# Performance work log

Hardware: AMD Instinct MI355X
Metric: run time of the kernel (lower is better)

## Reference

```python
import jax, jax.numpy as jnp
import numpy as np

N_NODES = 50000
N_EDGES = 800000
IN_C, HID_C, OUT_C = 128, 128, 64


def setup_inputs() -> dict:
    key = jax.random.key(0)
    ks = jax.random.split(key, 12)
    glorot = lambda k, shape: jax.random.normal(k, shape, dtype=jnp.float32) * (2.0 / (shape[0] + shape[-1])) ** 0.5
    return {
        "x": jax.random.normal(ks[0], (N_NODES, IN_C), dtype=jnp.float32),
        "edge_index": jax.random.randint(ks[1], (2, N_EDGES), 0, N_NODES, dtype=jnp.int64),
        "W_s1": glorot(ks[2], (IN_C, HID_C)), "b_s1": jnp.zeros((HID_C,), jnp.float32),
        "W_s2": glorot(ks[3], (HID_C, HID_C)), "b_s2": jnp.zeros((HID_C,), jnp.float32),
        "W_m1": glorot(ks[4], (IN_C, HID_C)), "b_m1": jnp.zeros((HID_C,), jnp.float32),
        "W_m21": glorot(ks[5], (IN_C, HID_C)), "b_m21": jnp.zeros((HID_C,), jnp.float32),
        "W_m22": glorot(ks[6], (HID_C, HID_C)), "b_m22": jnp.zeros((HID_C,), jnp.float32),
        "W_att": glorot(ks[7], (HID_C, 1)), "b_att": jnp.zeros((1,), jnp.float32),
        "W_fc": glorot(ks[8], (2 * HID_C, OUT_C)), "b_fc": jnp.zeros((OUT_C,), jnp.float32),
    }


def _gcn_conv(x, W, b, src, dst, n_nodes):
    """PyG GCNConv: add self-loops, symmetric deg^-1/2 norm, linear, scatter-add, bias."""
    xw = x @ W  # [N, H]
    loop = jnp.arange(n_nodes, dtype=src.dtype)
    s = jnp.concatenate([src, loop])
    d = jnp.concatenate([dst, loop])
    ones = jnp.ones(s.shape[0], dtype=x.dtype)
    deg = jax.ops.segment_sum(ones, d, num_segments=n_nodes)  # in-degree incl. self loop
    dinv = jnp.where(deg > 0, jax.lax.rsqrt(deg), 0.0)
    norm = dinv[s] * dinv[d]  # [E+N]
    msg = xw[s] * norm[:, None]
    return jax.ops.segment_sum(msg, d, num_segments=n_nodes) + b


def reference(x, edge_index, W_s1, b_s1, W_s2, b_s2, W_m1, b_m1, W_m21, b_m21,
              W_m22, b_m22, W_att, b_att, W_fc, b_fc):
    n = x.shape[0]
    src, dst = edge_index[0], edge_index[1]
    # structural branch: two GCN layers
    h_struct = jax.nn.relu(_gcn_conv(x, W_s1, b_s1, src, dst, n))
    h_struct = jax.nn.relu(_gcn_conv(h_struct, W_s2, b_s2, src, dst, n))
    # meta branches
    h1 = jax.nn.relu(_gcn_conv(x, W_m1, b_m1, src, dst, n))
    h2 = jax.nn.relu(_gcn_conv(x, W_m21, b_m21, src, dst, n))
    h2 = jax.nn.relu(_gcn_conv(h2, W_m22, b_m22, src, dst, n))
    # attention-weighted fusion over the 2 branches
    H = jnp.stack([h1, h2], axis=1)  # [N, 2, H]
    attn_scores = H @ W_att + b_att  # [N, 2, 1]
    attn_weights = jax.nn.softmax(attn_scores, axis=1)
    h_meta = jnp.sum(attn_weights * H, axis=1)  # [N, H]
    h_comb = jnp.concatenate([h_struct, h_meta], axis=1)  # [N, 2H]
    return h_comb @ W_fc + b_fc  # [N, OUT_C]
```

## Files before the change

### kernel.cpp

```cpp
#include <hip/hip_runtime.h>
#include <hip/hip_bf16.h>

#define N_NODES 50000
#define N_EDGES 800000
#define IN_C 128
#define HID_C 128
#define OUT_C 64

#define SCAN_BS 256
#define SCAN_NB ((N_NODES + SCAN_BS - 1) / SCAN_BS)

#define PREP_CVT_NB   6250
#define PREP_DEG_NB   3125
#define PREP_WCAT_NB  192
#define PREP_TP_NB    64
#define PREP_NB (PREP_CVT_NB + PREP_DEG_NB + PREP_WCAT_NB + 3 * PREP_TP_NB)

typedef __attribute__((ext_vector_type(8))) short bf16x8;
typedef __attribute__((ext_vector_type(4))) float f32x4;

__device__ __forceinline__ ushort f2bf(float f) {
    unsigned u = __float_as_uint(f);
    return (ushort)((u + 0x7fffu + ((u >> 16) & 1u)) >> 16);
}
__device__ __forceinline__ float bf2f(ushort u) {
    return __uint_as_float(((unsigned)u) << 16);
}

__global__ __launch_bounds__(256)
void prep_kernel(const float* __restrict__ x, uint2* __restrict__ xb4,
                 const int* __restrict__ edst, int* __restrict__ hist,
                 const float* __restrict__ Ws1, const float* __restrict__ Wm21,
                 const float* __restrict__ Wm1,
                 const float* __restrict__ bs1, const float* __restrict__ bm21,
                 const float* __restrict__ bm1,
                 ushort* __restrict__ Wcat_t, float* __restrict__ bcat,
                 const float* __restrict__ Ws2, ushort* __restrict__ Ws2t,
                 const float* __restrict__ Wm22, ushort* __restrict__ Wm22t,
                 const float* __restrict__ Wfc, ushort* __restrict__ Wfct,
                 int* __restrict__ row_ptr) {
    const int bid = blockIdx.x;
    const int t = threadIdx.x;
    if (bid < PREP_CVT_NB) {
        int i = bid * 256 + t;
        float4 v = *(const float4*)&x[(size_t)i * 4];
        uint2 o;
        o.x = (uint)f2bf(v.x) | ((uint)f2bf(v.y) << 16);
        o.y = (uint)f2bf(v.z) | ((uint)f2bf(v.w) << 16);
        xb4[i] = o;
    } else if (bid < PREP_CVT_NB + PREP_DEG_NB) {
        int e = (bid - PREP_CVT_NB) * 256 + t;
        atomicAdd(&hist[edst[e]], 1);
    } else if (bid < PREP_CVT_NB + PREP_DEG_NB + PREP_WCAT_NB) {
        int idx = (bid - PREP_CVT_NB - PREP_DEG_NB) * 256 + t;
        int c = idx >> 7, k = idx & 127;
        float v = (c < 128) ? Ws1[k * 128 + c]
                : (c < 256) ? Wm21[k * 128 + (c - 128)]
                            : Wm1[k * 128 + (c - 256)];
        Wcat_t[idx] = f2bf(v);
        if (idx < 384) {
            bcat[idx] = (idx < 128) ? bs1[idx] : (idx < 256) ? bm21[idx - 128] : bm1[idx - 256];
        }
        if (idx == 0) row_ptr[N_NODES] = N_EDGES;
    } else if (bid < PREP_CVT_NB + PREP_DEG_NB + PREP_WCAT_NB + PREP_TP_NB) {
        int idx = (bid - PREP_CVT_NB - PREP_DEG_NB - PREP_WCAT_NB) * 256 + t;
        int c = idx >> 7, k = idx & 127;
        Ws2t[idx] = f2bf(Ws2[(size_t)k * 128 + c]);
    } else if (bid < PREP_CVT_NB + PREP_DEG_NB + PREP_WCAT_NB + 2 * PREP_TP_NB) {
        int idx = (bid - PREP_CVT_NB - PREP_DEG_NB - PREP_WCAT_NB - PREP_TP_NB) * 256 + t;
        int c = idx >> 7, k = idx & 127;
        Wm22t[idx] = f2bf(Wm22[(size_t)k * 128 + c]);
    } else {
        int idx = (bid - PREP_CVT_NB - PREP_DEG_NB - PREP_WCAT_NB - 2 * PREP_TP_NB) * 256 + t;
        int c = idx >> 8, k = idx & 255;
        Wfct[idx] = f2bf(Wfc[(size_t)k * 64 + c]);
    }
}

__global__ __launch_bounds__(SCAN_BS)
void scan1_kernel(const int* __restrict__ hist, int* __restrict__ bsum,
                  float* __restrict__ dinv, int n) {
    __shared__ int s[SCAN_BS];
    int t = threadIdx.x;
    int i = blockIdx.x * SCAN_BS + t;
    int v = (i < n) ? hist[i] : 0;
    if (i < n) dinv[i] = rsqrtf((float)(v + 1));
    s[t] = v;
    __syncthreads();
#pragma unroll
    for (int off = SCAN_BS / 2; off > 0; off >>= 1) {
        if (t < off) s[t] += s[t + off];
        __syncthreads();
    }
    if (t == 0) bsum[blockIdx.x] = s[0];
}

__global__ __launch_bounds__(SCAN_BS)
void scan3_kernel(const int* __restrict__ hist, const int* __restrict__ bsum,
                  int* __restrict__ row_ptr, int* __restrict__ cursor, int n) {
    __shared__ int s[SCAN_BS];
    __shared__ int pre_s;
    int t = threadIdx.x;
    int b = blockIdx.x;
    int p = 0;
    for (int j = t; j < b; j += SCAN_BS) p += bsum[j];
    s[t] = p;
    __syncthreads();
#pragma unroll
    for (int off = SCAN_BS / 2; off > 0; off >>= 1) {
        if (t < off) s[t] += s[t + off];
        __syncthreads();
    }
    if (t == 0) pre_s = s[0];
    __syncthreads();
    const int pre = pre_s;
    __syncthreads();
    int i = b * SCAN_BS + t;
    int v = (i < n) ? hist[i] : 0;
    s[t] = v;
    __syncthreads();
#pragma unroll
    for (int off = 1; off < SCAN_BS; off <<= 1) {
        int tmp = (t >= off) ? s[t - off] : 0;
        __syncthreads();
        s[t] += tmp;
        __syncthreads();
    }
    if (i < n) {
        int ex = s[t] - v + pre;
        row_ptr[i] = ex;
        cursor[i]  = ex;
    }
}

__global__ void fill_kernel(const int* __restrict__ src, const int* __restrict__ dst, int E,
                            int* __restrict__ cursor, int2* __restrict__ edge_data,
                            const float* __restrict__ dinv) {
    int e = blockIdx.x * blockDim.x + threadIdx.x;
    if (e < E) {
        int d = dst[e];
        int s = src[e];
        int pos = atomicAdd(&cursor[d], 1);
        edge_data[pos] = make_int2(s, __float_as_int(dinv[s]));
    }
}

template<int C>
__global__ __launch_bounds__(256)
void agg_bf16(const ushort* __restrict__ X, int ldx,
              ushort* __restrict__ Y, int ldy,
              const int* __restrict__ row_ptr,
              const int2* __restrict__ edge_data,
              const float* __restrict__ dinv, int n) {
    constexpr int CG = C / 8;
    constexpr int SLOTS = 64 / CG;
    const int wid = blockIdx.x * (blockDim.x >> 6) + (threadIdx.x >> 6);
    if (wid >= n) return;
    const int lane = threadIdx.x & 63;
    const int cg = lane & (CG - 1);
    const int slot = lane / CG;

    const float di = dinv[wid];
    float acc[8] = {0.f, 0.f, 0.f, 0.f, 0.f, 0.f, 0.f, 0.f};

    auto fma_row = [&](uint4 v, float w) {
        acc[0] = fmaf(w, __uint_as_float(v.x << 16), acc[0]);
        acc[1] = fmaf(w, __uint_as_float(v.x & 0xffff0000u), acc[1]);
        acc[2] = fmaf(w, __uint_as_float(v.y << 16), acc[2]);
        acc[3] = fmaf(w, __uint_as_float(v.y & 0xffff0000u), acc[3]);
        acc[4] = fmaf(w, __uint_as_float(v.z << 16), acc[4]);
        acc[5] = fmaf(w, __uint_as_float(v.z & 0xffff0000u), acc[5]);
        acc[6] = fmaf(w, __uint_as_float(v.w << 16), acc[6]);
        acc[7] = fmaf(w, __uint_as_float(v.w & 0xffff0000u), acc[7]);
    };

    if (slot == 0) {
        uint4 v = *(const uint4*)&X[(size_t)wid * ldx + cg * 8];
        fma_row(v, di * di);
    }
    const int e0 = row_ptr[wid], e1 = row_ptr[wid + 1];
    int e = e0 + slot;
    for (; e + 3 * SLOTS < e1; e += 4 * SLOTS) {
        const int2 d0 = edge_data[e];
        const int2 d1 = edge_data[e + SLOTS];
        const int2 d2 = edge_data[e + 2 * SLOTS];
        const int2 d3 = edge_data[e + 3 * SLOTS];
        const uint4 v0 = *(const uint4*)&X[(size_t)d0.x * ldx + cg * 8];
        const uint4 v1 = *(const uint4*)&X[(size_t)d1.x * ldx + cg * 8];
        const uint4 v2 = *(const uint4*)&X[(size_t)d2.x * ldx + cg * 8];
        const uint4 v3 = *(const uint4*)&X[(size_t)d3.x * ldx + cg * 8];
        fma_row(v0, di * __int_as_float(d0.y));
        fma_row(v1, di * __int_as_float(d1.y));
        fma_row(v2, di * __int_as_float(d2.y));
        fma_row(v3, di * __int_as_float(d3.y));
    }
    for (; e < e1; e += SLOTS) {
        const int2 d0 = edge_data[e];
        const uint4 v0 = *(const uint4*)&X[(size_t)d0.x * ldx + cg * 8];
        fma_row(v0, di * __int_as_float(d0.y));
    }
#pragma unroll
    for (int j = 0; j < 8; ++j) {
        if (SLOTS == 4) acc[j] += __shfl_xor(acc[j], 16);
        if (SLOTS >= 2) acc[j] += __shfl_xor(acc[j], 32);
    }
    if (slot == 0) {
        uint4 o;
        o.x = (uint)f2bf(acc[0]) | ((uint)f2bf(acc[1]) << 16);
        o.y = (uint)f2bf(acc[2]) | ((uint)f2bf(acc[3]) << 16);
        o.z = (uint)f2bf(acc[4]) | ((uint)f2bf(acc[5]) << 16);
        o.w = (uint)f2bf(acc[6]) | ((uint)f2bf(acc[7]) << 16);
        *(uint4*)&Y[(size_t)wid * ldy + cg * 8] = o;
    }
}

__global__ __launch_bounds__(256)
void mfma_gemm_kernel(const ushort* __restrict__ A, int lda,
                      const ushort* __restrict__ Wt,
                      const float* __restrict__ bias,
                      void* __restrict__ Yv, int ldy,
                      int M, int relu, int obf16) {
    __shared__ char Asmem[128 * 272];
    const int tid = threadIdx.x;
    const int lane = tid & 63;
    const int w = tid >> 6;
    const int rb = blockIdx.x * 128;
    const int cb = blockIdx.y * 128;

    {
        const int rowbase = tid >> 4;
        const int inrow = (tid & 15) * 8;
#pragma unroll
        for (int it = 0; it < 8; ++it) {
            int row = it * 16 + rowbase;
            uint4 v = make_uint4(0u, 0u, 0u, 0u);
            int r = rb + row;
            if (r < M) v = *(const uint4*)&A[(size_t)r * lda + inrow];
            *(uint4*)&Asmem[row * 272 + (tid & 15) * 16] = v;
        }
    }
    __syncthreads();

    f32x4 acc[2][8];
#pragma unroll
    for (int i = 0; i < 2; ++i)
#pragma unroll
        for (int j = 0; j < 8; ++j) acc[i][j] = (f32x4){0.f, 0.f, 0.f, 0.f};

    const int arow0 = w * 32 + (lane & 15);
    const int kq = (lane >> 4) * 8;
    const int ccol = lane & 15;
#pragma unroll
    for (int ks = 0; ks < 4; ++ks) {
        const int k0 = ks * 32;
        const bf16x8 a0 = *(const bf16x8*)&Asmem[arow0 * 272 + (k0 + kq) * 2];
        const bf16x8 a1 = *(const bf16x8*)&Asmem[(arow0 + 16) * 272 + (k0 + kq) * 2];
#pragma unroll
        for (int ct = 0; ct < 8; ++ct) {
            const bf16x8 b = *(const bf16x8*)&Wt[(size_t)(cb + ct * 16 + ccol) * 128 + k0 + kq];
            acc[0][ct] = __builtin_amdgcn_mfma_f32_16x16x32_bf16(a0, b, acc[0][ct], 0, 0, 0);
            acc[1][ct] = __builtin_amdgcn_mfma_f32_16x16x32_bf16(a1, b, acc[1][ct], 0, 0, 0);
        }
    }

    const int rowq = (lane >> 4) * 4;
#pragma unroll
    for (int rt = 0; rt < 2; ++rt) {
#pragma unroll
        for (int ct = 0; ct < 8; ++ct) {
            const int col = cb + ct * 16 + ccol;
            const float bcol = bias[col];
#pragma unroll
            for (int r = 0; r < 4; ++r) {
                const int row = rb + w * 32 + rt * 16 + rowq + r;
                if (row >= M) continue;
                float v = acc[rt][ct][r] + bcol;
                if (relu) v = fmaxf(v, 0.f);
                if (obf16) ((ushort*)Yv)[(size_t)row * ldy + col] = f2bf(v);
                else       ((float*)Yv)[(size_t)row * ldy + col] = v;
            }
        }
    }
}

__global__ __launch_bounds__(256)
void gemm2_kernel(const ushort* __restrict__ bufB,
                  const ushort* __restrict__ Ws2t, const float* __restrict__ bs2,
                  const ushort* __restrict__ Wm22t, const float* __restrict__ bm22,
                  const ushort* __restrict__ cat1,
                  const float* __restrict__ Watt, const float* __restrict__ batt,
                  ushort* __restrict__ comb, int M) {
    __shared__ char Asmem[128 * 272];
    const int tid = threadIdx.x;
    const int lane = tid & 63;
    const int w = tid >> 6;
    const int rb = blockIdx.x * 128;
    const int branch = blockIdx.y;
    const ushort* A = bufB + (branch ? 128 : 0);
    const ushort* Wt = branch ? Wm22t : Ws2t;
    const float* bias = branch ? bm22 : bs2;

    {
        const int rowbase = tid >> 4;
        const int seg = tid & 15;
#pragma unroll
        for (int it = 0; it < 8; ++it) {
            int row = it * 16 + rowbase;
            uint4 v = make_uint4(0u, 0u, 0u, 0u);
            int r = rb + row;
            if (r < M) v = *(const uint4*)&A[(size_t)r * 256 + seg * 8];
            *(uint4*)&Asmem[row * 272 + seg * 16] = v;
        }
    }
    __syncthreads();

    f32x4 acc[2][8];
#pragma unroll
    for (int i = 0; i < 2; ++i)
#pragma unroll
        for (int j = 0; j < 8; ++j) acc[i][j] = (f32x4){0.f, 0.f, 0.f, 0.f};

    const int arow0 = w * 32 + (lane & 15);
    const int kq = (lane >> 4) * 8;
    const int ccol = lane & 15;
#pragma unroll
    for (int ks = 0; ks < 4; ++ks) {
        const int k0 = ks * 32;
        const bf16x8 a0 = *(const bf16x8*)&Asmem[arow0 * 272 + (k0 + kq) * 2];
        const bf16x8 a1 = *(const bf16x8*)&Asmem[(arow0 + 16) * 272 + (k0 + kq) * 2];
#pragma unroll
        for (int ct = 0; ct < 8; ++ct) {
            const bf16x8 b = *(const bf16x8*)&Wt[(size_t)(ct * 16 + ccol) * 128 + k0 + kq];
            acc[0][ct] = __builtin_amdgcn_mfma_f32_16x16x32_bf16(a0, b, acc[0][ct], 0, 0, 0);
            acc[1][ct] = __builtin_amdgcn_mfma_f32_16x16x32_bf16(a1, b, acc[1][ct], 0, 0, 0);
        }
    }

    const int quad = lane >> 4;
    if (branch == 0) {
#pragma unroll
        for (int rt = 0; rt < 2; ++rt) {
#pragma unroll
            for (int ct = 0; ct < 8; ++ct) {
                const int col = ct * 16 + ccol;
                const float bcol = bias[col];
#pragma unroll
                for (int r = 0; r < 4; ++r) {
                    const int row = rb + w * 32 + rt * 16 + quad * 4 + r;
                    if (row >= M) continue;
                    comb[(size_t)row * 256 + col] = f2bf(fmaxf(acc[rt][ct][r] + bcol, 0.f));
                }
            }
        }
    } else {
#pragma unroll
        for (int rt = 0; rt < 2; ++rt)
#pragma unroll
            for (int ct = 0; ct < 8; ++ct) {
                const float bcol = bias[ct * 16 + ccol];
#pragma unroll
                for (int r = 0; r < 4; ++r)
                    acc[rt][ct][r] = fmaxf(acc[rt][ct][r] + bcol, 0.f);
            }
        float wv[8];
#pragma unroll
        for (int ct = 0; ct < 8; ++ct) wv[ct] = Watt[ct * 16 + ccol];
        const float ba = batt[0];
#pragma unroll
        for (int rt = 0; rt < 2; ++rt) {
#pragma unroll
            for (int r = 0; r < 4; ++r) {
                const int row0 = rb + w * 32 + rt * 16 + quad * 4 + r;
                const int rowc = (row0 < M) ? row0 : (M - 1);
                const ushort* h1row = &cat1[(size_t)rowc * 384 + 256];
                float bp = 0.f, ap = 0.f;
#pragma unroll
                for (int ct = 0; ct < 8; ++ct) {
                    bp += acc[rt][ct][r] * wv[ct];
                    ap += bf2f(h1row[ct * 16 + ccol]) * wv[ct];
                }
#pragma unroll
                for (int off = 1; off < 16; off <<= 1) {
                    bp += __shfl_xor(bp, off);
                    ap += __shfl_xor(ap, off);
                }
                const float a = ap + ba, b = bp + ba;
                const float m = fmaxf(a, b);
                const float ea = __expf(a - m), eb = __expf(b - m);
                const float inv = 1.f / (ea + eb);
                const float wa = ea * inv, wb = eb * inv;
                if (row0 < M) {
#pragma unroll
                    for (int ct = 0; ct < 8; ++ct) {
                        const float h1 = bf2f(h1row[ct * 16 + ccol]);
                        comb[(size_t)row0 * 256 + 128 + ct * 16 + ccol] =
                            f2bf(fmaf(wa, h1, wb * acc[rt][ct][r]));
                    }
                }
            }
        }
    }
}

__global__ __launch_bounds__(256)
void mfma_fc_kernel(const ushort* __restrict__ A,
                    const ushort* __restrict__ Wt,
                    const float* __restrict__ bias,
                    float* __restrict__ Y, int M) {
    __shared__ char Asmem[64 * 528];
    const int tid = threadIdx.x;
    const int lane = tid & 63;
    const int w = tid >> 6;
    const int rb = blockIdx.x * 64;

    {
        const int rowbase = tid >> 5;
        const int seg = (tid & 31);
#pragma unroll
        for (int it = 0; it < 8; ++it) {
            int row = it * 8 + rowbase;
            uint4 v = make_uint4(0u, 0u, 0u, 0u);
            int r = rb + row;
            if (r < M) v = *(const uint4*)&A[(size_t)r * 256 + seg * 8];
            *(uint4*)&Asmem[row * 528 + seg * 16] = v;
        }
    }
    __syncthreads();

    f32x4 acc[4];
#pragma unroll
    for (int j = 0; j < 4; ++j) acc[j] = (f32x4){0.f, 0.f, 0.f, 0.f};

    const int arow = w * 16 + (lane & 15);
    const int kq = (lane >> 4) * 8;
    const int ccol = lane & 15;
#pragma unroll
    for (int ks = 0; ks < 8; ++ks) {
        const int k0 = ks * 32;
        const bf16x8 a = *(const bf16x8*)&Asmem[arow * 528 + (k0 + kq) * 2];
#pragma unroll
        for (int ct = 0; ct < 4; ++ct) {
            const bf16x8 b = *(const bf16x8*)&Wt[(size_t)(ct * 16 + ccol) * 256 + k0 + kq];
            acc[ct] = __builtin_amdgcn_mfma_f32_16x16x32_bf16(a, b, acc[ct], 0, 0, 0);
        }
    }

    const int rowq = (lane >> 4) * 4;
#pragma unroll
    for (int ct = 0; ct < 4; ++ct) {
        const int col = ct * 16 + ccol;
        const float bcol = bias[col];
#pragma unroll
        for (int r = 0; r < 4; ++r) {
            const int row = rb + w * 16 + rowq + r;
            if (row < M) Y[(size_t)row * 64 + col] = acc[ct][r] + bcol;
        }
    }
}

extern "C" void kernel_launch(void* const* d_in, const int* in_sizes, int n_in,
                              void* d_out, int out_size, void* d_ws, size_t ws_size,
                              hipStream_t stream) {
    const int N = N_NODES, E = N_EDGES;
    const float* x     = (const float*)d_in[0];
    const int*   ei    = (const int*)d_in[1];
    const int*   esrc  = ei;
    const int*   edst  = ei + E;
    const float* W_s1  = (const float*)d_in[2];
    const float* b_s1  = (const float*)d_in[3];
    const float* W_s2  = (const float*)d_in[4];
    const float* b_s2  = (const float*)d_in[5];
    const float* W_m1  = (const float*)d_in[6];
    const float* b_m1  = (const float*)d_in[7];
    const float* W_m21 = (const float*)d_in[8];
    const float* b_m21 = (const float*)d_in[9];
    const float* W_m22 = (const float*)d_in[10];
    const float* b_m22 = (const float*)d_in[11];
    const float* W_att = (const float*)d_in[12];
    const float* b_att = (const float*)d_in[13];
    const float* W_fc  = (const float*)d_in[14];
    const float* b_fc  = (const float*)d_in[15];
    float* out = (float*)d_out;

    char* base = (char*)d_ws;
    size_t off = 0;
    auto take = [&](size_t nbytes) -> void* {
        void* p = base + off;
        off += (nbytes + 255) & ~(size_t)255;
        return p;
    };
    int*    hist      = (int*)take((size_t)N * 4);
    int*    cursor    = (int*)take((size_t)N * 4);
    int*    row_ptr   = (int*)take((size_t)(N + 1) * 4);
    int*    bsum      = (int*)take((size_t)SCAN_NB * 4);
    int2*   edge_data = (int2*)take((size_t)E * 8);
    float*  dinv      = (float*)take((size_t)N * 4);
    ushort* xb        = (ushort*)take((size_t)N * 128 * 2);
    ushort* agg_x     = (ushort*)take((size_t)N * 128 * 2);
    ushort* cat1      = (ushort*)take((size_t)N * 384 * 2);
    ushort* bufB      = (ushort*)take((size_t)N * 256 * 2);
    ushort* comb      = (ushort*)take((size_t)N * 256 * 2);
    ushort* Wcat_t    = (ushort*)take((size_t)384 * 128 * 2);
    ushort* Ws2_t     = (ushort*)take((size_t)128 * 128 * 2);
    ushort* Wm22_t    = (ushort*)take((size_t)128 * 128 * 2);
    ushort* Wfc_t     = (ushort*)take((size_t)64 * 256 * 2);
    float*  bcat      = (float*)take((size_t)384 * 4);

    hipMemsetAsync(hist, 0, (size_t)N * 4, stream);
    prep_kernel<<<PREP_NB, 256, 0, stream>>>(x, (uint2*)xb, edst, hist,
                                             W_s1, W_m21, W_m1, b_s1, b_m21, b_m1,
                                             Wcat_t, bcat, W_s2, Ws2_t, W_m22, Wm22_t,
                                             W_fc, Wfc_t, row_ptr);
    scan1_kernel<<<SCAN_NB, SCAN_BS, 0, stream>>>(hist, bsum, dinv, N);
    scan3_kernel<<<SCAN_NB, SCAN_BS, 0, stream>>>(hist, bsum, row_ptr, cursor, N);
    fill_kernel<<<(E + 255) / 256, 256, 0, stream>>>(esrc, edst, E, cursor, edge_data, dinv);

    agg_bf16<128><<<(N + 3) / 4, 256, 0, stream>>>(xb, 128, agg_x, 128, row_ptr, edge_data, dinv, N);
    dim3 gm384((N + 127) / 128, 3);
    mfma_gemm_kernel<<<gm384, 256, 0, stream>>>(agg_x, 128, Wcat_t, bcat, cat1, 384, N, 1, 1);
    agg_bf16<256><<<(N + 3) / 4, 256, 0, stream>>>(cat1, 384, bufB, 256, row_ptr, edge_data, dinv, N);
    dim3 gm2((N + 127) / 128, 2);
    gemm2_kernel<<<gm2, 256, 0, stream>>>(bufB, Ws2_t, b_s2, Wm22_t, b_m22,
                                          cat1, W_att, b_att, comb, N);
    mfma_fc_kernel<<<(N + 63) / 64, 256, 0, stream>>>(comb, Wfc_t, b_fc, out, N);
}
```

Before: 383.6 us.

## Fuse second-layer GEMMs, attention fusion and final FC into one kernel

Merges the two-branch second GEMM (with attention softmax fusion) and the final FC GEMM into a single 512-thread kernel. The combined bf16 activations stay in shared memory instead of being written to and re-read from a global comb buffer, which also removes one kernel launch. Each block now handles both branches with 8 waves and uses about 68KB of LDS, which lowers occupancy. The mfma_gemm kernel is also simplified to hardcode relu and bf16 output.

```diff
diff --git a/kernel.cpp b/kernel.cpp
--- a/kernel.cpp
+++ b/kernel.cpp
@@ -3,9 +3,6 @@
 
 #define N_NODES 50000
 #define N_EDGES 800000
-#define IN_C 128
-#define HID_C 128
-#define OUT_C 64
 
 #define SCAN_BS 256
 #define SCAN_NB ((N_NODES + SCAN_BS - 1) / SCAN_BS)
@@ -218,8 +215,7 @@
 void mfma_gemm_kernel(const ushort* __restrict__ A, int lda,
                       const ushort* __restrict__ Wt,
                       const float* __restrict__ bias,
-                      void* __restrict__ Yv, int ldy,
-                      int M, int relu, int obf16) {
+                      ushort* __restrict__ Y, int ldy, int M) {
     __shared__ char Asmem[128 * 272];
     const int tid = threadIdx.x;
     const int lane = tid & 63;
@@ -229,14 +225,14 @@
 
     {
         const int rowbase = tid >> 4;
-        const int inrow = (tid & 15) * 8;
+        const int seg = tid & 15;
 #pragma unroll
         for (int it = 0; it < 8; ++it) {
             int row = it * 16 + rowbase;
             uint4 v = make_uint4(0u, 0u, 0u, 0u);
             int r = rb + row;
-            if (r < M) v = *(const uint4*)&A[(size_t)r * lda + inrow];
-            *(uint4*)&Asmem[row * 272 + (tid & 15) * 16] = v;
+            if (r < M) v = *(const uint4*)&A[(size_t)r * lda + seg * 8];
+            *(uint4*)&Asmem[row * 272 + seg * 16] = v;
         }
     }
     __syncthreads();
@@ -274,60 +270,62 @@
             for (int r = 0; r < 4; ++r) {
                 const int row = rb + w * 32 + rt * 16 + rowq + r;
                 if (row >= M) continue;
-                float v = acc[rt][ct][r] + bcol;
-                if (relu) v = fmaxf(v, 0.f);
-                if (obf16) ((ushort*)Yv)[(size_t)row * ldy + col] = f2bf(v);
-                else       ((float*)Yv)[(size_t)row * ldy + col] = v;
+                Y[(size_t)row * ldy + col] = f2bf(fmaxf(acc[rt][ct][r] + bcol, 0.f));
             }
         }
     }
 }
 
-__global__ __launch_bounds__(256)
-void gemm2_kernel(const ushort* __restrict__ bufB,
-                  const ushort* __restrict__ Ws2t, const float* __restrict__ bs2,
-                  const ushort* __restrict__ Wm22t, const float* __restrict__ bm22,
-                  const ushort* __restrict__ cat1,
-                  const float* __restrict__ Watt, const float* __restrict__ batt,
-                  ushort* __restrict__ comb, int M) {
-    __shared__ char Asmem[128 * 272];
+__global__ __launch_bounds__(512, 4)
+void gemm2fc_kernel(const ushort* __restrict__ bufB,
+                    const ushort* __restrict__ Ws2t, const float* __restrict__ bs2,
+                    const ushort* __restrict__ Wm22t, const float* __restrict__ bm22,
+                    const ushort* __restrict__ cat1,
+                    const float* __restrict__ Watt, const float* __restrict__ batt,
+                    const ushort* __restrict__ Wfct, const float* __restrict__ bfc,
+                    float* __restrict__ Y, int M) {
+    __shared__ __align__(16) char smem[69632];
     const int tid = threadIdx.x;
+    const int rb = blockIdx.x * 128;
+
+    {
+        const int seg = tid & 15;
+        const int rowbase = tid >> 4;
+#pragma unroll
+        for (int it = 0; it < 8; ++it) {
+            int idx = it * 32 + rowbase;
+            int region = idx >> 7;
+            int row = idx & 127;
+            int r = rb + row;
+            uint4 v = make_uint4(0u, 0u, 0u, 0u);
+            if (r < M) v = *(const uint4*)&bufB[(size_t)r * 256 + region * 128 + seg * 8];
+            *(uint4*)&smem[region * 34816 + row * 272 + seg * 16] = v;
+        }
+    }
+    __syncthreads();
+
+    const int w = tid >> 6;
     const int lane = tid & 63;
-    const int w = tid >> 6;
-    const int rb = blockIdx.x * 128;
-    const int branch = blockIdx.y;
-    const ushort* A = bufB + (branch ? 128 : 0);
+    const int branch = w >> 2;
+    const int wl = w & 3;
+    const char* Areg = smem + branch * 34816;
     const ushort* Wt = branch ? Wm22t : Ws2t;
     const float* bias = branch ? bm22 : bs2;
 
-    {
-        const int rowbase = tid >> 4;
-        const int seg = tid & 15;
-#pragma unroll
-        for (int it = 0; it < 8; ++it) {
-            int row = it * 16 + rowbase;
-            uint4 v = make_uint4(0u, 0u, 0u, 0u);
-            int r = rb + row;
-            if (r < M) v = *(const uint4*)&A[(size_t)r * 256 + seg * 8];
-            *(uint4*)&Asmem[row * 272 + seg * 16] = v;
-        }
-    }
-    __syncthreads();
-
     f32x4 acc[2][8];
 #pragma unroll
     for (int i = 0; i < 2; ++i)
 #pragma unroll
         for (int j = 0; j < 8; ++j) acc[i][j] = (f32x4){0.f, 0.f, 0.f, 0.f};
 
-    const int arow0 = w * 32 + (lane & 15);
+    const int arow0 = wl * 32 + (lane & 15);
     const int kq = (lane >> 4) * 8;
     const int ccol = lane & 15;
 #pragma unroll
     for (int ks = 0; ks < 4; ++ks) {
         const int k0 = ks * 32;
-        const bf16x8 a0 = *(const bf16x8*)&Asmem[arow0 * 272 + (k0 + kq) * 2];
-        const bf16x8 a1 = *(const bf16x8*)&Asmem[(arow0 + 16) * 272 + (k0 + kq) * 2];
+        const bf16x8 a0 = *(const bf16x8*)&Areg[arow0 * 272 + (k0 + kq) * 2];
+        const bf16x8 a1 = *(const bf16x8*)&Areg[(arow0 + 16) * 272 + (k0 + kq) * 2];
 #pragma unroll
         for (int ct = 0; ct < 8; ++ct) {
             const bf16x8 b = *(const bf16x8*)&Wt[(size_t)(ct * 16 + ccol) * 128 + k0 + kq];
@@ -336,32 +334,18 @@
         }
     }
 
+#pragma unroll
+    for (int rt = 0; rt < 2; ++rt)
+#pragma unroll
+        for (int ct = 0; ct < 8; ++ct) {
+            const float bcol = bias[ct * 16 + ccol];
+#pragma unroll
+            for (int r = 0; r < 4; ++r)
+                acc[rt][ct][r] = fmaxf(acc[rt][ct][r] + bcol, 0.f);
+        }
+
     const int quad = lane >> 4;
-    if (branch == 0) {
-#pragma unroll
-        for (int rt = 0; rt < 2; ++rt) {
-#pragma unroll
-            for (int ct = 0; ct < 8; ++ct) {
-                const int col = ct * 16 + ccol;
-                const float bcol = bias[col];
-#pragma unroll
-                for (int r = 0; r < 4; ++r) {
-                    const int row = rb + w * 32 + rt * 16 + quad * 4 + r;
-                    if (row >= M) continue;
-                    comb[(size_t)row * 256 + col] = f2bf(fmaxf(acc[rt][ct][r] + bcol, 0.f));
-                }
-            }
-        }
-    } else {
-#pragma unroll
-        for (int rt = 0; rt < 2; ++rt)
-#pragma unroll
-            for (int ct = 0; ct < 8; ++ct) {
-                const float bcol = bias[ct * 16 + ccol];
-#pragma unroll
-                for (int r = 0; r < 4; ++r)
-                    acc[rt][ct][r] = fmaxf(acc[rt][ct][r] + bcol, 0.f);
-            }
+    if (branch == 1) {
         float wv[8];
 #pragma unroll
         for (int ct = 0; ct < 8; ++ct) wv[ct] = Watt[ct * 16 + ccol];
@@ -370,7 +354,7 @@
         for (int rt = 0; rt < 2; ++rt) {
 #pragma unroll
             for (int r = 0; r < 4; ++r) {
-                const int row0 = rb + w * 32 + rt * 16 + quad * 4 + r;
+                const int row0 = rb + wl * 32 + rt * 16 + quad * 4 + r;
                 const int rowc = (row0 < M) ? row0 : (M - 1);
                 const ushort* h1row = &cat1[(size_t)rowc * 384 + 256];
                 float bp = 0.f, ap = 0.f;
@@ -389,71 +373,52 @@
                 const float ea = __expf(a - m), eb = __expf(b - m);
                 const float inv = 1.f / (ea + eb);
                 const float wa = ea * inv, wb = eb * inv;
-                if (row0 < M) {
-#pragma unroll
-                    for (int ct = 0; ct < 8; ++ct) {
-                        const float h1 = bf2f(h1row[ct * 16 + ccol]);
-                        comb[(size_t)row0 * 256 + 128 + ct * 16 + ccol] =
-                            f2bf(fmaf(wa, h1, wb * acc[rt][ct][r]));
-                    }
+#pragma unroll
+                for (int ct = 0; ct < 8; ++ct) {
+                    const float h1 = bf2f(h1row[ct * 16 + ccol]);
+                    acc[rt][ct][r] = fmaf(wa, h1, wb * acc[rt][ct][r]);
                 }
             }
         }
     }
-}
-
-__global__ __launch_bounds__(256)
-void mfma_fc_kernel(const ushort* __restrict__ A,
-                    const ushort* __restrict__ Wt,
-                    const float* __restrict__ bias,
-                    float* __restrict__ Y, int M) {
-    __shared__ char Asmem[64 * 528];
-    const int tid = threadIdx.x;
-    const int lane = tid & 63;
-    const int w = tid >> 6;
-    const int rb = blockIdx.x * 64;
-
-    {
-        const int rowbase = tid >> 5;
-        const int seg = (tid & 31);
-#pragma unroll
-        for (int it = 0; it < 8; ++it) {
-            int row = it * 8 + rowbase;
-            uint4 v = make_uint4(0u, 0u, 0u, 0u);
-            int r = rb + row;
-            if (r < M) v = *(const uint4*)&A[(size_t)r * 256 + seg * 8];
-            *(uint4*)&Asmem[row * 528 + seg * 16] = v;
-        }
-    }
-    __syncthreads();
-
-    f32x4 acc[4];
-#pragma unroll
-    for (int j = 0; j < 4; ++j) acc[j] = (f32x4){0.f, 0.f, 0.f, 0.f};
-
-    const int arow = w * 16 + (lane & 15);
-    const int kq = (lane >> 4) * 8;
-    const int ccol = lane & 15;
+    __syncthreads();
+
+#pragma unroll
+    for (int rt = 0; rt < 2; ++rt) {
+#pragma unroll
+        for (int ct = 0; ct < 8; ++ct) {
+            const int col = branch * 128 + ct * 16 + ccol;
+#pragma unroll
+            for (int r = 0; r < 4; ++r) {
+                const int row = wl * 32 + rt * 16 + quad * 4 + r;
+                *(ushort*)&smem[row * 528 + col * 2] = f2bf(acc[rt][ct][r]);
+            }
+        }
+    }
+    __syncthreads();
+
+    f32x4 fcacc[4];
+#pragma unroll
+    for (int j = 0; j < 4; ++j) fcacc[j] = (f32x4){0.f, 0.f, 0.f, 0.f};
+    const int frow = w * 16 + (lane & 15);
 #pragma unroll
     for (int ks = 0; ks < 8; ++ks) {
         const int k0 = ks * 32;
-        const bf16x8 a = *(const bf16x8*)&Asmem[arow * 528 + (k0 + kq) * 2];
+        const bf16x8 a = *(const bf16x8*)&smem[frow * 528 + (k0 + kq) * 2];
 #pragma unroll
         for (int ct = 0; ct < 4; ++ct) {
-            const bf16x8 b = *(const bf16x8*)&Wt[(size_t)(ct * 16 + ccol) * 256 + k0 + kq];
-            acc[ct] = __builtin_amdgcn_mfma_f32_16x16x32_bf16(a, b, acc[ct], 0, 0, 0);
-        }
-    }
-
-    const int rowq = (lane >> 4) * 4;
+            const bf16x8 b = *(const bf16x8*)&Wfct[(size_t)(ct * 16 + ccol) * 256 + k0 + kq];
+            fcacc[ct] = __builtin_amdgcn_mfma_f32_16x16x32_bf16(a, b, fcacc[ct], 0, 0, 0);
+        }
+    }
 #pragma unroll
     for (int ct = 0; ct < 4; ++ct) {
         const int col = ct * 16 + ccol;
-        const float bcol = bias[col];
+        const float bcol = bfc[col];
 #pragma unroll
         for (int r = 0; r < 4; ++r) {
-            const int row = rb + w * 16 + rowq + r;
-            if (row < M) Y[(size_t)row * 64 + col] = acc[ct][r] + bcol;
+            const int row = rb + w * 16 + quad * 4 + r;
+            if (row < M) Y[(size_t)row * 64 + col] = fcacc[ct][r] + bcol;
         }
     }
 }
@@ -499,7 +464,6 @@
     ushort* agg_x     = (ushort*)take((size_t)N * 128 * 2);
     ushort* cat1      = (ushort*)take((size_t)N * 384 * 2);
     ushort* bufB      = (ushort*)take((size_t)N * 256 * 2);
-    ushort* comb      = (ushort*)take((size_t)N * 256 * 2);
     ushort* Wcat_t    = (ushort*)take((size_t)384 * 128 * 2);
     ushort* Ws2_t     = (ushort*)take((size_t)128 * 128 * 2);
     ushort* Wm22_t    = (ushort*)take((size_t)128 * 128 * 2);
@@ -517,10 +481,8 @@
 
     agg_bf16<128><<<(N + 3) / 4, 256, 0, stream>>>(xb, 128, agg_x, 128, row_ptr, edge_data, dinv, N);
     dim3 gm384((N + 127) / 128, 3);
-    mfma_gemm_kernel<<<gm384, 256, 0, stream>>>(agg_x, 128, Wcat_t, bcat, cat1, 384, N, 1, 1);
+    mfma_gemm_kernel<<<gm384, 256, 0, stream>>>(agg_x, 128, Wcat_t, bcat, cat1, 384, N);
     agg_bf16<256><<<(N + 3) / 4, 256, 0, stream>>>(cat1, 384, bufB, 256, row_ptr, edge_data, dinv, N);
-    dim3 gm2((N + 127) / 128, 2);
-    gemm2_kernel<<<gm2, 256, 0, stream>>>(bufB, Ws2_t, b_s2, Wm22_t, b_m22,
-                                          cat1, W_att, b_att, comb, N);
-    mfma_fc_kernel<<<(N + 63) / 64, 256, 0, stream>>>(comb, Wfc_t, b_fc, out, N);
-}
+    gemm2fc_kernel<<<(N + 127) / 128, 512, 0, stream>>>(bufB, Ws2_t, b_s2, Wm22_t, b_m22,
+                                                        cat1, W_att, b_att, Wfc_t, b_fc, out, N);
+}
```

New measurement: 375.7 us. 1.02x faster.
